# Optimization experiments

Hardware: AMD Instinct MI355X
Metric: run time of the kernel (lower is better)

## Reference

```python
import jax, jax.numpy as jnp
import numpy as np

T, B, D, H = 512, 128, 512, 512

def setup_inputs() -> dict:
    key = jax.random.key(0)
    k1, k2, k3, k4 = jax.random.split(key, 4)
    s_in = 1.0 / np.sqrt(D)
    s_h = 1.0 / np.sqrt(H)
    return {
        "x": jax.random.normal(k1, (T, B, D), dtype=jnp.float32),
        "resets": jax.random.randint(k2, (T, B), 0, 2) > 0,
        "h0": jnp.zeros((B, H), dtype=jnp.float32),  # GRUCell.initialize_carry -> zeros
        "Wi": jax.random.normal(k3, (D, 3 * H), dtype=jnp.float32) * s_in,  # [ir|iz|in]
        "bi": jnp.zeros((3 * H,), dtype=jnp.float32),
        "Wh": jax.random.normal(k4, (H, 3 * H), dtype=jnp.float32) * s_h,  # [hr|hz|hn]
        "bhn": jnp.zeros((H,), dtype=jnp.float32),
    }

def reference(x, resets, h0, Wi, bi, Wh, bhn):
    # Precompute all input-side gate projections in one big GEMM: [T,B,3H]
    xg = jnp.einsum('tbd,dk->tbk', x, Wi) + bi

    def step(h, inp):
        xg_t, reset_t = inp
        # reset masking: replace carry with fresh zero carry where episode resets
        h = jnp.where(reset_t[:, None], jnp.zeros_like(h), h)
        hg = h @ Wh  # [B,3H]
        xr, xz, xn = jnp.split(xg_t, 3, axis=-1)
        hr, hz, hn = jnp.split(hg, 3, axis=-1)
        r = jax.nn.sigmoid(xr + hr)
        z = jax.nn.sigmoid(xz + hz)
        n = jnp.tanh(xn + r * (hn + bhn))
        h_new = (1.0 - z) * n + z * h
        return h_new, h_new

    h_final, ys = jax.lax.scan(step, h0, (xg, resets))
    return h_final, ys
```

## Files before the change

### kernel.cpp

```cpp
#include <hip/hip_runtime.h>

typedef __attribute__((ext_vector_type(4))) float f32x4;
typedef __attribute__((ext_vector_type(8))) _Float16 f16x8;
typedef __attribute__((ext_vector_type(4))) _Float16 f16x4;
typedef unsigned short u16;
typedef unsigned int u32;

#define XGCAP 36864

__device__ __forceinline__ float sigm(float v){ return 1.0f / (1.0f + __expf(-v)); }
__device__ __forceinline__ float tanh_fast(float v){
  v = fminf(15.0f, fmaxf(-15.0f, v));
  float e = __expf(2.0f * v);
  return (e - 1.0f) / (e + 1.0f);
}
__device__ __forceinline__ void gload16(const void* g, void* l){
  __builtin_amdgcn_global_load_lds((const __attribute__((address_space(1))) void*)g,
                                   (__attribute__((address_space(3))) void*)l, 16, 0, 0);
}
__device__ __forceinline__ double aload(const double* p){
  return __hip_atomic_load(p, __ATOMIC_RELAXED, __HIP_MEMORY_SCOPE_AGENT);
}
__device__ __forceinline__ void astore(float* p, float v){
  __hip_atomic_store(p, v, __ATOMIC_RELAXED, __HIP_MEMORY_SCOPE_AGENT);
}
__device__ __forceinline__ float2 d2f2(double d){ union{double d; float2 f;} u; u.d = d; return u.f; }

__global__ void prep_lists(const void* __restrict__ resets_raw,
                           u32* __restrict__ rows, u32* __restrict__ off,
                           int* __restrict__ nlists)
{
  __shared__ u32 cnt[520];
  __shared__ u32 offs[521];
  __shared__ int is_bytes;
  const int tid = threadIdx.x;
  for (int i = tid; i < 520; i += 128) cnt[i] = 0;
  if (tid == 0) is_bytes = 0;
  for (int i = tid; i < 64; i += 128) rows[65536 + i] = (2u << 16);
  __syncthreads();
  {
    const u32* w = (const u32*)resets_raw;
    int bad = 0;
    for (int i = tid; i < 4096; i += 128) bad |= (w[i] > 1u);
    if (bad) atomicOr(&is_bytes, 1);
  }
  __syncthreads();
  const bool as_bytes = (is_bytes != 0);
  const u32* ri32 = (const u32*)resets_raw;
  const unsigned char* ru8 = (const unsigned char*)resets_raw;
  const int b = tid;
  {
    int depth = 0;
    for (int t = 0; t < 512; ++t){
      bool rs = as_bytes ? (ru8[t*128 + b] != 0) : (ri32[t*128 + b] != 0u);
      depth = rs ? 0 : ((t == 0) ? 0 : depth + 1);
      int li = (depth == 0) ? (rs ? 0 : 1) : (depth + 1);
      atomicAdd(&cnt[li], 1u);
    }
  }
  __syncthreads();
  if (tid == 0){
    u32 s = 0; int mx = 0;
    for (int i = 0; i < 520; ++i){
      offs[i] = s; s += cnt[i];
      if (cnt[i]) mx = i;
    }
    offs[520] = s;
    *nlists = mx + 1;
  }
  __syncthreads();
  for (int i = tid; i < 521; i += 128) off[i] = offs[i];
  for (int i = tid; i < 520; i += 128) cnt[i] = 0;
  __syncthreads();
  {
    int depth = 0;
    for (int t = 0; t < 512; ++t){
      bool rs = as_bytes ? (ru8[t*128 + b] != 0) : (ri32[t*128 + b] != 0u);
      depth = rs ? 0 : ((t == 0) ? 0 : depth + 1);
      int li = (depth == 0) ? (rs ? 0 : 1) : (depth + 1);
      u32 p = offs[li] + atomicAdd(&cnt[li], 1u);
      u32 fl = rs ? 1u : ((t == 0) ? 2u : 0u);
      rows[p] = (u32)t | ((u32)b << 9) | (fl << 16);
    }
  }
}

__global__ void prep_w(const float* __restrict__ Wi, const float* __restrict__ Wh,
                       char* __restrict__ wimg)
{
  __shared__ float tile[64][65];
  const int bc = blockIdx.x % 24;
  const int bk = blockIdx.x / 24;
  const int scol0 = (bc % 3) * 512 + (bc / 3) * 64;
  const int k0 = bk * 64;
  #pragma unroll
  for (int i = 0; i < 4; ++i){
    int idx = (int)threadIdx.x + i*256;
    int kk = idx >> 4, c4 = idx & 15;
    int k = k0 + kk;
    const float* src = (k < 512) ? (Wi + (size_t)k*1536 + scol0 + c4*4)
                                 : (Wh + (size_t)(k-512)*1536 + scol0 + c4*4);
    float4 v = *(const float4*)src;
    tile[kk][c4*4+0] = v.x; tile[kk][c4*4+1] = v.y;
    tile[kk][c4*4+2] = v.z; tile[kk][c4*4+3] = v.w;
  }
  __syncthreads();
  const int jb = bc / 3;
  #pragma unroll
  for (int i = 0; i < 4; ++i){
    int idx = (int)threadIdx.x + i*256;
    int cc = idx >> 4, k4 = idx & 15;
    int cimg = (bc % 3)*64 + cc;
    f16x4 c;
    c[0] = (_Float16)tile[k4*4+0][cc]; c[1] = (_Float16)tile[k4*4+1][cc];
    c[2] = (_Float16)tile[k4*4+2][cc]; c[3] = (_Float16)tile[k4*4+3][cc];
    int bby = k4*8;
    int sb = (bby & 8) | ((bby & 0x70) ^ ((cimg & 7) << 4));
    *(f16x4*)(wimg + ((size_t)(jb*16 + bk))*24576 + cimg*128 + sb) = c;
  }
}

__global__ __launch_bounds__(256, 2) void xg_gemm(
    const float* __restrict__ x, const float* __restrict__ bi,
    const float* __restrict__ bhn, const char* __restrict__ wimg,
    _Float16* __restrict__ xg, const u32* __restrict__ rows,
    const u32* __restrict__ off, u32* __restrict__ flags,
    float* __restrict__ out)
{
  __shared__ __align__(16) char smem[81920];
  const int tid = threadIdx.x;
  const int lane = tid & 63, wave = tid >> 6;
  const int tm = (int)blockIdx.x >> 3, jblk = (int)blockIdx.x & 7;
  float* ys = out + 65536;
  const u32 n0 = off[1];
  const size_t wbase = ((size_t)jblk*16)*24576;

  const float* rp[8];
  #pragma unroll
  for (int i = 0; i < 8; ++i){
    u32 e = rows[tm*128 + (tid>>4) + i*16];
    rp[i] = x + ((size_t)((e & 511u)*128u + ((e >> 9) & 127u)))*512 + (tid & 15)*4;
  }

  f32x4 acc[3][8];
  #pragma unroll
  for (int c = 0; c < 3; ++c)
    #pragma unroll
    for (int m = 0; m < 8; ++m) acc[c][m] = (f32x4){0.f,0.f,0.f,0.f};

  float4 areg[8];
  #pragma unroll
  for (int i = 0; i < 8; ++i) areg[i] = *(const float4*)(rp[i]);
  {
    const char* g = wimg + wbase + wave*6144 + lane*16;
    char* l = smem + 32768 + wave*6144;
    #pragma unroll
    for (int i = 0; i < 6; ++i) gload16(g + i*1024, l + i*1024);
  }
  #pragma unroll
  for (int i = 0; i < 8; ++i){
    int r = (tid>>4) + i*16, bby = (tid & 15)*8;
    int sb = (bby & 8) | ((bby & 0x70) ^ ((r & 7) << 4));
    f16x4 c; c[0]=(_Float16)areg[i].x; c[1]=(_Float16)areg[i].y;
             c[2]=(_Float16)areg[i].z; c[3]=(_Float16)areg[i].w;
    *(f16x4*)(smem + r*128 + sb) = c;
  }
  __syncthreads();

  for (int kc = 0; kc < 8; ++kc){
    const int cur = kc & 1;
    if (kc < 7){
      #pragma unroll
      for (int i = 0; i < 8; ++i) areg[i] = *(const float4*)(rp[i] + (kc+1)*64);
      const char* g = wimg + wbase + (size_t)(kc+1)*24576 + wave*6144 + lane*16;
      char* l = smem + 32768 + ((kc+1)&1)*24576 + wave*6144;
      #pragma unroll
      for (int i = 0; i < 6; ++i) gload16(g + i*1024, l + i*1024);
    }
    const char* Ab = smem + cur*16384;
    const char* Wb = smem + 32768 + cur*24576;
    #pragma unroll
    for (int kk = 0; kk < 2; ++kk){
      const int bby = kk*64 + (lane>>4)*16;
      f16x8 af[8];
      #pragma unroll
      for (int mi = 0; mi < 8; ++mi){
        int rr = mi*16 + (lane & 15);
        af[mi] = *(const f16x8*)(Ab + rr*128 + (bby ^ ((rr & 7) << 4)));
      }
      #pragma unroll
      for (int cls = 0; cls < 3; ++cls){
        int cc = cls*64 + wave*16 + (lane & 15);
        f16x8 wf = *(const f16x8*)(Wb + cc*128 + (bby ^ ((cc & 7) << 4)));
        #pragma unroll
        for (int mi = 0; mi < 8; ++mi)
          acc[cls][mi] = __builtin_amdgcn_mfma_f32_16x16x32_f16(af[mi], wf, acc[cls][mi], 0, 0, 0);
      }
    }
    if (kc < 7){
      char* An = smem + ((kc+1)&1)*16384;
      #pragma unroll
      for (int i = 0; i < 8; ++i){
        int r = (tid>>4) + i*16, bby = (tid & 15)*8;
        int sb = (bby & 8) | ((bby & 0x70) ^ ((r & 7) << 4));
        f16x4 c; c[0]=(_Float16)areg[i].x; c[1]=(_Float16)areg[i].y;
                 c[2]=(_Float16)areg[i].z; c[3]=(_Float16)areg[i].w;
        *(f16x4*)(An + r*128 + sb) = c;
      }
    }
    __syncthreads();
  }

  const int jloc = wave*16 + (lane & 15);
  const int j = jblk*64 + jloc;
  const float bir = bi[j], biz = bi[512 + j], bin = bi[1024 + j], bh = bhn[j];
  #pragma unroll
  for (int mi = 0; mi < 8; ++mi){
    #pragma unroll
    for (int rg = 0; rg < 4; ++rg){
      int r = mi*16 + (lane >> 4)*4 + rg;
      u32 e = rows[tm*128 + r];
      int tt = (int)(e & 511u), bb = (int)((e >> 9) & 127u);
      float xr = acc[0][mi][rg] + bir;
      float xz = acc[1][mi][rg] + biz;
      float xn = acc[2][mi][rg] + bin;
      if ((e >> 16) == 1u){
        float rr = sigm(xr), zz = sigm(xz);
        float nn = tanh_fast(xn + rr*bh);
        ys[((size_t)(tt*128 + bb))*512 + j] = (1.f - zz)*nn;
      } else {
        u32 xi = (u32)(tm*128 + r) - n0;
        if (xi >= XGCAP) xi = 0;
        _Float16* p = xg + (size_t)xi*1536 + jblk*192 + jloc;
        p[0]   = (_Float16)xr;
        p[64]  = (_Float16)xz;
        p[128] = (_Float16)xn;
      }
    }
  }
  __syncthreads();
  if (tid < 128){
    u32 e = rows[tm*128 + tid];
    if ((e >> 16) == 1u){
      u32 fidx = (e & 511u)*128u + ((e >> 9) & 127u);
      __hip_atomic_fetch_add(&flags[fidx], 1u, __ATOMIC_RELAXED, __HIP_MEMORY_SCOPE_AGENT);
    }
  }
}

__global__ __launch_bounds__(256, 2) void gru_scan(
    const float* __restrict__ h0, const float* __restrict__ bhn,
    const char* __restrict__ wimg, const _Float16* __restrict__ xg,
    const u32* __restrict__ rows, const u32* __restrict__ off,
    const int* __restrict__ nlists, u32* __restrict__ flags,
    float* __restrict__ out)
{
  __shared__ __align__(16) char smem[32768];
  float* ys = out + 65536;
  const int L = *nlists;
  const u32 n0 = off[1];
  const int tid = threadIdx.x;
  const int lane = tid & 63, wave = tid >> 6;
  const int nblk = (int)gridDim.x;

  int myNext = (int)blockIdx.x;
  int gt = 0;
  for (int li = 1; li < L; ++li){
    const u32 offA = off[li];
    const int nA = (int)(off[li+1] - offA);
    const int tA = (nA + 63) >> 6;
    const int nt = tA * 8;
    while (myNext < gt + nt){
      const int tile = myNext - gt;
      myNext += nblk;
      const int tm = tile >> 3, jb = tile & 7;
      const u32 rowbase = offA + (u32)tm*64u;
      const int mcount = min(64, nA - tm*64);
      const char* wp = wimg + ((size_t)jb*16 + 8)*24576;

      if (wave == 0){
        u32 e = rows[rowbase + lane];
        if (lane < mcount && (e >> 16) == 0u){
          u32 fidx = ((e & 511u) - 1u)*128u + ((e >> 9) & 127u);
          int guard = 0;
          while (__hip_atomic_load(&flags[fidx], __ATOMIC_RELAXED, __HIP_MEMORY_SCOPE_AGENT) < 8u){
            __builtin_amdgcn_s_sleep(1);
            if (++guard > (1 << 20)) break;
          }
        }
      }
      __syncthreads();

      const float* rp[4];
      #pragma unroll
      for (int i = 0; i < 4; ++i){
        u32 e = rows[rowbase + (tid>>4) + i*16];
        int tt = (int)(e & 511u), bb = (int)((e >> 9) & 127u);
        const float* base = ((e >> 16) == 0u) ? (ys + ((size_t)((tt-1)*128 + bb))*512)
                                              : (h0 + (size_t)bb*512);
        rp[i] = base + (tid & 15)*4;
      }

      f32x4 acc[3][4];
      #pragma unroll
      for (int c = 0; c < 3; ++c)
        #pragma unroll
        for (int m = 0; m < 4; ++m) acc[c][m] = (f32x4){0.f,0.f,0.f,0.f};
      float hp[4][4];
      double s0[4][2], s1[4][2], s2[4][2];

#define ALOAD(S, CK) do{ \
    _Pragma("unroll") for (int i_ = 0; i_ < 4; ++i_){ \
      const double* p_ = (const double*)(rp[i_] + (CK)*64); \
      S[i_][0] = aload(p_); S[i_][1] = aload(p_ + 1); } }while(0)

#define AWRITE(S, CK) do{ \
    char* An_ = smem + ((CK) & 3)*8192; \
    _Pragma("unroll") for (int i_ = 0; i_ < 4; ++i_){ \
      float2 u0_ = d2f2(S[i_][0]), u1_ = d2f2(S[i_][1]); \
      int r_ = (tid>>4) + i_*16, bby_ = (tid & 15)*8; \
      int sb_ = (bby_ & 8) | ((bby_ & 0x70) ^ ((r_ & 7) << 4)); \
      f16x4 c_; c_[0]=(_Float16)u0_.x; c_[1]=(_Float16)u0_.y; \
                c_[2]=(_Float16)u1_.x; c_[3]=(_Float16)u1_.y; \
      *(f16x4*)(An_ + r_*128 + sb_) = c_; } }while(0)

#define COMPUTE(KC) do{ \
    const char* Ab_ = smem + ((KC) & 3)*8192; \
    _Pragma("unroll") for (int kk_ = 0; kk_ < 2; ++kk_){ \
      const int bby_ = kk_*64 + (lane>>4)*16; \
      f16x8 af_[4]; \
      _Pragma("unroll") for (int mi_ = 0; mi_ < 4; ++mi_){ \
        int rr_ = mi_*16 + (lane & 15); \
        af_[mi_] = *(const f16x8*)(Ab_ + rr_*128 + (bby_ ^ ((rr_ & 7) << 4))); } \
      _Pragma("unroll") for (int cl_ = 0; cl_ < 3; ++cl_){ \
        int cc_ = cl_*64 + wave*16 + (lane & 15); \
        f16x8 wf_ = *(const f16x8*)(wp + (size_t)(KC)*24576 + cc_*128 + (bby_ ^ ((cc_ & 7) << 4))); \
        _Pragma("unroll") for (int mi_ = 0; mi_ < 4; ++mi_) \
          acc[cl_][mi_] = __builtin_amdgcn_mfma_f32_16x16x32_f16(af_[mi_], wf_, acc[cl_][mi_], 0, 0, 0); } } \
    if ((KC) == jb){ \
      const int jl_ = wave*16 + (lane & 15); \
      const int bb2_ = jl_*2; \
      _Pragma("unroll") for (int mi_ = 0; mi_ < 4; ++mi_) \
        _Pragma("unroll") for (int rg_ = 0; rg_ < 4; ++rg_){ \
          int r2_ = mi_*16 + (lane >> 4)*4 + rg_; \
          int sb2_ = (bb2_ & 0x0F) | ((bb2_ & 0x70) ^ ((r2_ & 7) << 4)); \
          hp[mi_][rg_] = (float)(*(const _Float16*)(Ab_ + r2_*128 + sb2_)); } } }while(0)

      ALOAD(s0, 0); ALOAD(s1, 1); ALOAD(s2, 2);
      AWRITE(s0, 0);
      __syncthreads();
      ALOAD(s0, 3); COMPUTE(0); AWRITE(s1, 1); __syncthreads();
      ALOAD(s1, 4); COMPUTE(1); AWRITE(s2, 2); __syncthreads();
      ALOAD(s2, 5); COMPUTE(2); AWRITE(s0, 3); __syncthreads();
      ALOAD(s0, 6); COMPUTE(3); AWRITE(s1, 4); __syncthreads();
      ALOAD(s1, 7); COMPUTE(4); AWRITE(s2, 5); __syncthreads();
                    COMPUTE(5); AWRITE(s0, 6); __syncthreads();
                    COMPUTE(6); AWRITE(s1, 7); __syncthreads();
                    COMPUTE(7);
#undef ALOAD
#undef AWRITE
#undef COMPUTE

      const int jloc = wave*16 + (lane & 15);
      const int j = jb*64 + jloc;
      const float bh = bhn[j];
      #pragma unroll
      for (int mi = 0; mi < 4; ++mi){
        #pragma unroll
        for (int rg = 0; rg < 4; ++rg){
          int r = mi*16 + (lane >> 4)*4 + rg;
          if (r < mcount){
            u32 lpos = rowbase + r;
            u32 e = rows[lpos];
            int tt = (int)(e & 511u), bb = (int)((e >> 9) & 127u);
            u32 xi = lpos - n0;
            if (xi >= XGCAP) xi = 0;
            const _Float16* p = xg + (size_t)xi*1536 + jb*192 + jloc;
            float rr = sigm((float)p[0]   + acc[0][mi][rg]);
            float zz = sigm((float)p[64]  + acc[1][mi][rg]);
            float nn = tanh_fast((float)p[128] + rr*(acc[2][mi][rg] + bh));
            astore(&ys[((size_t)(tt*128 + bb))*512 + j], (1.f - zz)*nn + zz*hp[mi][rg]);
          }
        }
      }
      __syncthreads();
      if (tid < mcount){
        u32 e = rows[rowbase + tid];
        u32 fidx = (e & 511u)*128u + ((e >> 9) & 127u);
        __hip_atomic_fetch_add(&flags[fidx], 1u, __ATOMIC_RELAXED, __HIP_MEMORY_SCOPE_AGENT);
      }
    }
    gt += nt;
  }

  for (int v = (int)blockIdx.x; v < 512; v += nblk){
    const int b = v & 127, jq = v >> 7;
    if (tid == 0){
      int guard = 0;
      while (__hip_atomic_load(&flags[511*128 + b], __ATOMIC_RELAXED, __HIP_MEMORY_SCOPE_AGENT) < 8u){
        __builtin_amdgcn_s_sleep(1);
        if (++guard > (1 << 20)) break;
      }
    }
    __syncthreads();
    if (tid < 128){
      const float* src = &ys[((size_t)(511*128 + b))*512 + jq*128 + tid];
      float val;
      {
        val = __hip_atomic_load(src, __ATOMIC_RELAXED, __HIP_MEMORY_SCOPE_AGENT);
      }
      out[(size_t)b*512 + jq*128 + tid] = val;
    }
    __syncthreads();
  }
}

extern "C" void kernel_launch(void* const* d_in, const int* in_sizes, int n_in,
                              void* d_out, int out_size, void* d_ws, size_t ws_size,
                              hipStream_t stream)
{
  const float* x  = (const float*)d_in[0];
  const void*  resets = d_in[1];
  const float* h0 = (const float*)d_in[2];
  const float* Wi = (const float*)d_in[3];
  const float* bi = (const float*)d_in[4];
  const float* Wh = (const float*)d_in[5];
  const float* bhn= (const float*)d_in[6];
  float* out = (float*)d_out;

  char* ws = (char*)d_ws;
  u32* off    = (u32*)ws;
  int* nlists = (int*)(ws + 4096);
  u32* rows   = (u32*)(ws + 8192);
  u32* flags  = (u32*)(ws + 294912);
  char* wimg  = ws + 589824;
  _Float16* xg = (_Float16*)(ws + 4194304);

  hipMemsetAsync(flags, 0, 65536*sizeof(u32), stream);
  prep_lists<<<dim3(1), dim3(128), 0, stream>>>(resets, rows, off, nlists);
  prep_w<<<dim3(384), dim3(256), 0, stream>>>(Wi, Wh, wimg);
  xg_gemm<<<dim3(4096), dim3(256), 0, stream>>>(x, bi, bhn, wimg, xg, rows, off, flags, out);

  int perCU = 0;
  (void)hipOccupancyMaxActiveBlocksPerMultiprocessor(&perCU, gru_scan, 256, 0);
  if (perCU < 1) perCU = 1;
  int grid = perCU * 256;
  if (grid > 1024) grid = 1024;

  void* args[] = {(void*)&h0, (void*)&bhn, (void*)&wimg, (void*)&xg,
                  (void*)&rows, (void*)&off, (void*)&nlists, (void*)&flags, (void*)&out};
  hipLaunchCooperativeKernel(gru_scan, dim3(grid), dim3(256), args, 0, stream);

  (void)in_sizes; (void)n_in; (void)out_size; (void)ws_size;
}
```

Measured before the change: 1.151 ms.

## Bitmap resets in prep_lists, prefetch xg gates, and swizzle xg_gemm block order

```diff
diff --git a/kernel.cpp b/kernel.cpp
--- a/kernel.cpp
+++ b/kernel.cpp
@@ -5,6 +5,7 @@
 typedef __attribute__((ext_vector_type(4))) _Float16 f16x4;
 typedef unsigned short u16;
 typedef unsigned int u32;
+typedef unsigned long long u64;
 
 #define XGCAP 36864
 
@@ -26,33 +27,56 @@
 }
 __device__ __forceinline__ float2 d2f2(double d){ union{double d; float2 f;} u; u.d = d; return u.f; }
 
-__global__ void prep_lists(const void* __restrict__ resets_raw,
-                           u32* __restrict__ rows, u32* __restrict__ off,
-                           int* __restrict__ nlists)
+__global__ __launch_bounds__(512) void prep_lists(
+    const void* __restrict__ resets_raw,
+    u32* __restrict__ rows, u32* __restrict__ off, int* __restrict__ nlists)
 {
+  __shared__ u32 bitmap[2048];
   __shared__ u32 cnt[520];
   __shared__ u32 offs[521];
+  __shared__ u32 cur[520];
   __shared__ int is_bytes;
   const int tid = threadIdx.x;
-  for (int i = tid; i < 520; i += 128) cnt[i] = 0;
+  const int lane = tid & 63, wave = tid >> 6;
+  for (int i = tid; i < 2048; i += 512) bitmap[i] = 0;
+  for (int i = tid; i < 520; i += 512){ cnt[i] = 0; cur[i] = 0; }
   if (tid == 0) is_bytes = 0;
-  for (int i = tid; i < 64; i += 128) rows[65536 + i] = (2u << 16);
+  for (int i = tid; i < 64; i += 512) rows[65536 + i] = (2u << 16);
   __syncthreads();
   {
     const u32* w = (const u32*)resets_raw;
     int bad = 0;
-    for (int i = tid; i < 4096; i += 128) bad |= (w[i] > 1u);
+    for (int i = tid; i < 4096; i += 512) bad |= (w[i] > 1u);
     if (bad) atomicOr(&is_bytes, 1);
   }
   __syncthreads();
-  const bool as_bytes = (is_bytes != 0);
-  const u32* ri32 = (const u32*)resets_raw;
-  const unsigned char* ru8 = (const unsigned char*)resets_raw;
-  const int b = tid;
-  {
+  if (is_bytes){
+    const u32* wb = (const u32*)resets_raw;
+    for (int i = tid; i < 16384; i += 512){
+      u32 v = wb[i];
+      u32 bits = ((v & 0xFFu) ? 1u : 0u) | (((v >> 8) & 0xFFu) ? 2u : 0u)
+               | (((v >> 16) & 0xFFu) ? 4u : 0u) | (((v >> 24) & 0xFFu) ? 8u : 0u);
+      if (bits) atomicOr(&bitmap[i >> 3], bits << ((i & 7) * 4));
+    }
+  } else {
+    const u32* w = (const u32*)resets_raw;
+    for (int r = 0; r < 128; ++r){
+      u32 v = w[r * 512 + tid];
+      u64 m = __ballot(v != 0u);
+      if (lane == 0){
+        int idx = r * 16 + wave * 2;
+        bitmap[idx]     = (u32)m;
+        bitmap[idx + 1] = (u32)(m >> 32);
+      }
+    }
+  }
+  __syncthreads();
+  if (tid < 128){
+    const int b = tid;
     int depth = 0;
     for (int t = 0; t < 512; ++t){
-      bool rs = as_bytes ? (ru8[t*128 + b] != 0) : (ri32[t*128 + b] != 0u);
+      int pos = t * 128 + b;
+      bool rs = (bitmap[pos >> 5] >> (pos & 31)) & 1u;
       depth = rs ? 0 : ((t == 0) ? 0 : depth + 1);
       int li = (depth == 0) ? (rs ? 0 : 1) : (depth + 1);
       atomicAdd(&cnt[li], 1u);
@@ -69,16 +93,17 @@
     *nlists = mx + 1;
   }
   __syncthreads();
-  for (int i = tid; i < 521; i += 128) off[i] = offs[i];
-  for (int i = tid; i < 520; i += 128) cnt[i] = 0;
-  __syncthreads();
-  {
+  for (int i = tid; i < 521; i += 512) off[i] = offs[i];
+  __syncthreads();
+  if (tid < 128){
+    const int b = tid;
     int depth = 0;
     for (int t = 0; t < 512; ++t){
-      bool rs = as_bytes ? (ru8[t*128 + b] != 0) : (ri32[t*128 + b] != 0u);
+      int pos = t * 128 + b;
+      bool rs = (bitmap[pos >> 5] >> (pos & 31)) & 1u;
       depth = rs ? 0 : ((t == 0) ? 0 : depth + 1);
       int li = (depth == 0) ? (rs ? 0 : 1) : (depth + 1);
-      u32 p = offs[li] + atomicAdd(&cnt[li], 1u);
+      u32 p = offs[li] + atomicAdd(&cur[li], 1u);
       u32 fl = rs ? 1u : ((t == 0) ? 2u : 0u);
       rows[p] = (u32)t | ((u32)b << 9) | (fl << 16);
     }
@@ -130,7 +155,10 @@
   __shared__ __align__(16) char smem[81920];
   const int tid = threadIdx.x;
   const int lane = tid & 63, wave = tid >> 6;
-  const int tm = (int)blockIdx.x >> 3, jblk = (int)blockIdx.x & 7;
+  const int c_  = (int)blockIdx.x & 7;
+  const int q_  = (int)blockIdx.x >> 3;
+  const int jblk = q_ & 7;
+  const int tm = c_ + ((q_ >> 3) << 3);
   float* ys = out + 65536;
   const u32 n0 = off[1];
   const size_t wbase = ((size_t)jblk*16)*24576;
@@ -277,6 +305,7 @@
       const u32 rowbase = offA + (u32)tm*64u;
       const int mcount = min(64, nA - tm*64);
       const char* wp = wimg + ((size_t)jb*16 + 8)*24576;
+      const int jloc = wave*16 + (lane & 15);
 
       if (wave == 0){
         u32 e = rows[rowbase + lane];
@@ -299,6 +328,21 @@
         const float* base = ((e >> 16) == 0u) ? (ys + ((size_t)((tt-1)*128 + bb))*512)
                                               : (h0 + (size_t)bb*512);
         rp[i] = base + (tid & 15)*4;
+      }
+
+      _Float16 xgp[3][4][4];
+      #pragma unroll
+      for (int mi = 0; mi < 4; ++mi){
+        #pragma unroll
+        for (int rg = 0; rg < 4; ++rg){
+          u32 lpos = rowbase + (u32)(mi*16 + (lane >> 4)*4 + rg);
+          u32 xi = lpos - n0;
+          if (xi >= XGCAP) xi = 0;
+          const _Float16* p = xg + (size_t)xi*1536 + jb*192 + jloc;
+          xgp[0][mi][rg] = p[0];
+          xgp[1][mi][rg] = p[64];
+          xgp[2][mi][rg] = p[128];
+        }
       }
 
       f32x4 acc[3][4];
@@ -338,8 +382,7 @@
         _Pragma("unroll") for (int mi_ = 0; mi_ < 4; ++mi_) \
           acc[cl_][mi_] = __builtin_amdgcn_mfma_f32_16x16x32_f16(af_[mi_], wf_, acc[cl_][mi_], 0, 0, 0); } } \
     if ((KC) == jb){ \
-      const int jl_ = wave*16 + (lane & 15); \
-      const int bb2_ = jl_*2; \
+      const int bb2_ = jloc*2; \
       _Pragma("unroll") for (int mi_ = 0; mi_ < 4; ++mi_) \
         _Pragma("unroll") for (int rg_ = 0; rg_ < 4; ++rg_){ \
           int r2_ = mi_*16 + (lane >> 4)*4 + rg_; \
@@ -361,7 +404,6 @@
 #undef AWRITE
 #undef COMPUTE
 
-      const int jloc = wave*16 + (lane & 15);
       const int j = jb*64 + jloc;
       const float bh = bhn[j];
       #pragma unroll
@@ -370,15 +412,11 @@
         for (int rg = 0; rg < 4; ++rg){
           int r = mi*16 + (lane >> 4)*4 + rg;
           if (r < mcount){
-            u32 lpos = rowbase + r;
-            u32 e = rows[lpos];
+            u32 e = rows[rowbase + r];
             int tt = (int)(e & 511u), bb = (int)((e >> 9) & 127u);
-            u32 xi = lpos - n0;
-            if (xi >= XGCAP) xi = 0;
-            const _Float16* p = xg + (size_t)xi*1536 + jb*192 + jloc;
-            float rr = sigm((float)p[0]   + acc[0][mi][rg]);
-            float zz = sigm((float)p[64]  + acc[1][mi][rg]);
-            float nn = tanh_fast((float)p[128] + rr*(acc[2][mi][rg] + bh));
+            float rr = sigm((float)xgp[0][mi][rg] + acc[0][mi][rg]);
+            float zz = sigm((float)xgp[1][mi][rg] + acc[1][mi][rg]);
+            float nn = tanh_fast((float)xgp[2][mi][rg] + rr*(acc[2][mi][rg] + bh));
             astore(&ys[((size_t)(tt*128 + bb))*512 + j], (1.f - zz)*nn + zz*hp[mi][rg]);
           }
         }
@@ -405,10 +443,7 @@
     __syncthreads();
     if (tid < 128){
       const float* src = &ys[((size_t)(511*128 + b))*512 + jq*128 + tid];
-      float val;
-      {
-        val = __hip_atomic_load(src, __ATOMIC_RELAXED, __HIP_MEMORY_SCOPE_AGENT);
-      }
+      float val = __hip_atomic_load(src, __ATOMIC_RELAXED, __HIP_MEMORY_SCOPE_AGENT);
       out[(size_t)b*512 + jq*128 + tid] = val;
     }
     __syncthreads();
@@ -437,7 +472,7 @@
   _Float16* xg = (_Float16*)(ws + 4194304);
 
   hipMemsetAsync(flags, 0, 65536*sizeof(u32), stream);
-  prep_lists<<<dim3(1), dim3(128), 0, stream>>>(resets, rows, off, nlists);
+  prep_lists<<<dim3(1), dim3(512), 0, stream>>>(resets, rows, off, nlists);
   prep_w<<<dim3(384), dim3(256), 0, stream>>>(Wi, Wh, wimg);
   xg_gemm<<<dim3(4096), dim3(256), 0, stream>>>(x, bi, bhn, wimg, xg, rows, off, flags, out);
 
```

After: 921.4 us. 1.25x faster.
